# Kernel optimization log

Hardware: AMD Instinct MI355X
Metric: run time of the kernel (lower is better)

The kernel has to match this reference:

```python
import jax, jax.numpy as jnp
import numpy as np

TOP_K = 4
NORM_TOPK_PROB = False  # Qwen2-MoE default

def setup_inputs() -> dict:
    key = jax.random.key(0)
    ks = jax.random.split(key, 10)
    B, S, D = 1, 2048, 2048
    E, F, FS = 8, 1408, 5632
    s = 0.02
    return {
        "hidden_states": jax.random.normal(ks[0], (B, S, D), jnp.float32),
        "gate_w": jax.random.normal(ks[1], (E, D), jnp.float32) * s,          # router Linear weight [E, D]
        "Wg": jax.random.normal(ks[2], (E, D, F), jnp.float32) * s,           # expert gate_proj
        "Wu": jax.random.normal(ks[3], (E, D, F), jnp.float32) * s,           # expert up_proj
        "Wd": jax.random.normal(ks[4], (E, F, D), jnp.float32) * s,           # expert down_proj
        "Wsg": jax.random.normal(ks[5], (D, FS), jnp.float32) * s,            # shared gate_proj
        "Wsu": jax.random.normal(ks[6], (D, FS), jnp.float32) * s,            # shared up_proj
        "Wsd": jax.random.normal(ks[7], (FS, D), jnp.float32) * s,            # shared down_proj
        "shared_gate_w": jax.random.normal(ks[8], (D, 1), jnp.float32) * s,   # shared_expert_gate Linear(D,1)
    }

def reference(hidden_states, gate_w, Wg, Wu, Wd, Wsg, Wsu, Wsd, shared_gate_w):
    B, S, D = hidden_states.shape
    x = hidden_states.reshape(-1, D)                       # [T, D]
    T = x.shape[0]
    router_logits = x @ gate_w.T                           # [T, E]
    probs = jax.nn.softmax(router_logits.astype(jnp.float32), axis=-1)
    top_vals, top_idx = jax.lax.top_k(probs, TOP_K)        # [T, K]
    if NORM_TOPK_PROB:
        top_vals = top_vals / jnp.sum(top_vals, axis=-1, keepdims=True)
    # dense routing-weight matrix: zero for unselected experts (same math as masked naive loop)
    w = jnp.zeros_like(probs).at[jnp.arange(T)[:, None], top_idx].set(top_vals)
    w = w.astype(x.dtype)                                  # [T, E]
    # per-expert SiLU-gated MLP, computed densely over all experts
    h = jax.nn.silu(jnp.einsum('td,edf->etf', x, Wg)) * jnp.einsum('td,edf->etf', x, Wu)  # [E, T, F]
    expert_out = jnp.einsum('etf,efd->etd', h, Wd)         # [E, T, D]
    moe_out = jnp.einsum('etd,te->td', expert_out, w)      # [T, D]
    # shared expert with sigmoid gate
    shared = (jax.nn.silu(x @ Wsg) * (x @ Wsu)) @ Wsd      # [T, D]
    shared = jax.nn.sigmoid(x @ shared_gate_w) * shared    # [T,1] * [T,D]
    out = (moe_out + shared).reshape(B, S, D)
    return out, router_logits
```

## Files before the change

### kernel.cpp

```cpp
#include <hip/hip_runtime.h>
#include <hip/hip_bf16.h>

typedef __attribute__((ext_vector_type(8))) __bf16 bf16x8;
typedef __attribute__((ext_vector_type(4))) float f32x4;

#define TKN 2048
#define DMODEL 2048
#define NEXP 8
#define FEXP 1408
#define FSH 5632

__device__ __forceinline__ unsigned short f2bf(float f) {
  unsigned u = __float_as_uint(f);
  u += 0x7FFFu + ((u >> 16) & 1u);
  return (unsigned short)(u >> 16);
}
__device__ __forceinline__ unsigned pk2(float a, float b) {
  return (unsigned)f2bf(a) | ((unsigned)f2bf(b) << 16);
}

__device__ __forceinline__ void gll16(const void* g, void* l) {
  __builtin_amdgcn_global_load_lds(
      (const __attribute__((address_space(1))) unsigned*)g,
      (__attribute__((address_space(3))) unsigned*)l, 16, 0, 0);
}

enum { EPI_GU = 0, EPI_DOWN = 1, EPI_SDOWN = 2 };

__global__ __launch_bounds__(256)
void router_k(const float* __restrict__ x, const float* __restrict__ gw,
              const float* __restrict__ sgw, float* __restrict__ logits,
              float* __restrict__ sig, int* __restrict__ cnt,
              int* __restrict__ tokl, float* __restrict__ wls)
{
  const int wv = threadIdx.x >> 6, lane = threadIdx.x & 63;
  const int t = blockIdx.x * 4 + wv;
  const float* xr = x + (long)t * DMODEL;
  float xv[32];
#pragma unroll
  for (int j = 0; j < 32; j++) xv[j] = xr[lane + (j << 6)];

  float lg[8];
#pragma unroll
  for (int e = 0; e < 8; e++) {
    const float* gr = gw + (long)e * DMODEL;
    float acc = 0.f;
#pragma unroll
    for (int j = 0; j < 32; j++) acc += xv[j] * gr[lane + (j << 6)];
#pragma unroll
    for (int s = 1; s < 64; s <<= 1) acc += __shfl_xor(acc, s, 64);
    lg[e] = acc;
  }
  float sgacc = 0.f;
#pragma unroll
  for (int j = 0; j < 32; j++) sgacc += xv[j] * sgw[lane + (j << 6)];
#pragma unroll
  for (int s = 1; s < 64; s <<= 1) sgacc += __shfl_xor(sgacc, s, 64);

  if (lane == 0) {
    float mx = lg[0];
#pragma unroll
    for (int e = 1; e < 8; e++) mx = fmaxf(mx, lg[e]);
    float p[8], se = 0.f;
#pragma unroll
    for (int e = 0; e < 8; e++) { p[e] = expf(lg[e] - mx); se += p[e]; }
    float inv = 1.f / se;
#pragma unroll
    for (int e = 0; e < 8; e++) { p[e] *= inv; logits[t * 8 + e] = lg[e]; }
    sig[t] = 1.f / (1.f + expf(-sgacc));
#pragma unroll
    for (int k = 0; k < 4; k++) {
      int bi = 0; float bv = p[0];
#pragma unroll
      for (int e = 1; e < 8; e++) if (p[e] > bv) { bv = p[e]; bi = e; }
      p[bi] = -1.f;
      int pos = atomicAdd(&cnt[bi], 1);
      tokl[bi * TKN + pos] = t;
      wls[bi * TKN + pos] = bv;
    }
  }
}

__global__ void scan_k(const int* __restrict__ cnt, int* __restrict__ offs) {
  if (threadIdx.x == 0) {
    int s = 0;
    for (int e = 0; e < 8; e++) { offs[e] = s; s += cnt[e]; }
    offs[8] = s;
  }
}

__global__ __launch_bounds__(256)
void cvt_x_k(const float* __restrict__ x, char* __restrict__ xbf)
{
  long id = (long)blockIdx.x * 256 + threadIdx.x;
  int row = id >> 8, u = id & 255, kt = u >> 2, j = u & 3;
  const float* p = x + (long)row * 2048 + kt * 32 + j * 4;
  float4 a = *(const float4*)p;
  float4 b = *(const float4*)(p + 16);
  uint4 o;
  o.x = pk2(a.x, a.y); o.y = pk2(a.z, a.w);
  o.z = pk2(b.x, b.y); o.w = pk2(b.z, b.w);
  *(uint4*)(xbf + id * 16) = o;
}

__global__ __launch_bounds__(256)
void cvt_w_k(const float* __restrict__ W, long sB, int N,
             char* __restrict__ panel, long panStride)
{
  const int ct = blockIdx.x, kt = blockIdx.y, e = blockIdx.z, KT = gridDim.y;
  const float* Wp = W + (long)e * sB + (long)(kt * 32) * N + ct * 128;
  __shared__ float t[32][128];
  const int r = threadIdx.x >> 3, q = threadIdx.x & 7;
  const float* rp = Wp + (long)r * N + q * 16;
  float4 f0 = *(const float4*)(rp + 0);
  float4 f1 = *(const float4*)(rp + 4);
  float4 f2 = *(const float4*)(rp + 8);
  float4 f3 = *(const float4*)(rp + 12);
  *(float4*)&t[r][q * 16 + 0]  = f0;
  *(float4*)&t[r][q * 16 + 4]  = f1;
  *(float4*)&t[r][q * 16 + 8]  = f2;
  *(float4*)&t[r][q * 16 + 12] = f3;
  __syncthreads();
  char* outp = panel + e * panStride + ((long)ct * KT + kt) * 8192;
#pragma unroll
  for (int uu = 0; uu < 2; uu++) {
    int u = threadIdx.x + uu * 256;
    int c = u >> 2, g = u & 3;
    uint4 o;
    o.x = pk2(t[g * 4 + 0][c], t[g * 4 + 1][c]);
    o.y = pk2(t[g * 4 + 2][c], t[g * 4 + 3][c]);
    o.z = pk2(t[16 + g * 4 + 0][c], t[16 + g * 4 + 1][c]);
    o.w = pk2(t[16 + g * 4 + 2][c], t[16 + g * 4 + 3][c]);
    *(uint4*)(outp + u * 16) = o;
  }
}

template<int EPI, bool EXPERT, int KSPLIT>
__global__ __launch_bounds__(256, 2)
void gemm2_k(const char* __restrict__ Abf, long strA,
             const char* __restrict__ Bp, const char* __restrict__ Bp2,
             long sBpan, int KTtot,
             void* __restrict__ O, int ldKo,
             const int* __restrict__ cnt, const int* __restrict__ offs,
             const int* __restrict__ tokl, const float* __restrict__ wls,
             const float* __restrict__ sig)
{
  constexpr bool FUSED = (EPI == EPI_GU);
  const int tid = threadIdx.x, lane = tid & 63, w = tid >> 6;

  int e = 0, rt, kc = 0, M = TKN;
  if (EXPERT) {
    e = blockIdx.y >> 4; rt = blockIdx.y & 15;
    M = cnt[e];
    if (rt * 128 >= M) return;
  } else {
    rt = blockIdx.y & 15; kc = blockIdx.y >> 4;
  }
  const int KT = KTtot / KSPLIT;
  const int kt0 = kc * KT;
  const int ct = blockIdx.x;
  const int obase = EXPERT ? offs[e] : 0;

  __shared__ int s_tok[128];
  __shared__ float s_w[128];
  __shared__ alignas(16) char Ab[2][8192];
  __shared__ alignas(16) char Bb[2][8192];
  __shared__ alignas(16) char Bb2[FUSED ? 2 : 1][FUSED ? 8192 : 16];

  if (EXPERT) {
    if (tid < 128) {
      int r = rt * 128 + tid;
      int rc = (r < M) ? r : (M - 1);
      s_tok[tid] = tokl[e * TKN + rc];
      if (EPI == EPI_DOWN) s_w[tid] = (r < M) ? wls[e * TKN + r] : 0.f;
    }
    __syncthreads();
  }

  const int lrow0 = w * 32 + (lane >> 2);
  const int lrow1 = lrow0 + 16;
  auto rowbyte = [&](int rl) -> long {
    long gr;
    if (EPI == EPI_DOWN) { int r = rt * 128 + rl; gr = obase + ((r < M) ? r : (M - 1)); }
    else if (EXPERT)     { gr = s_tok[rl]; }
    else                 { gr = rt * 128 + rl; }
    return gr * strA;
  };
  const char* gA0 = Abf + rowbyte(lrow0) + (long)kt0 * 64 + (lane & 3) * 16;
  const char* gA1 = Abf + rowbyte(lrow1) + (long)kt0 * 64 + (lane & 3) * 16;
  const long bbase = (EXPERT ? (long)e * sBpan : 0) + ((long)ct * KTtot + kt0) * 8192
                     + w * 2048 + (long)lane * 16;
  const char* gB  = Bp + bbase;
  const char* gB2 = FUSED ? (Bp2 + bbase) : nullptr;

  auto stage = [&](int bf, int kt) {
    long ao = (long)kt * 64, bo = (long)kt * 8192;
    gll16(gA0 + ao, &Ab[bf][w * 2048]);
    gll16(gA1 + ao, &Ab[bf][w * 2048 + 1024]);
    gll16(gB + bo, &Bb[bf][w * 2048]);
    gll16(gB + bo + 1024, &Bb[bf][w * 2048 + 1024]);
    if constexpr (FUSED) {
      gll16(gB2 + bo, &Bb2[bf][w * 2048]);
      gll16(gB2 + bo + 1024, &Bb2[bf][w * 2048 + 1024]);
    }
  };

  const int wm = w >> 1, wn = w & 1, g = lane >> 4, l15 = lane & 15;
  int raOff[4], rbOff[4];
#pragma unroll
  for (int m = 0; m < 4; m++) raOff[m] = (wm * 64 + m * 16 + l15) * 64 + g * 16;
#pragma unroll
  for (int n = 0; n < 4; n++) rbOff[n] = (wn * 64 + n * 16 + l15) * 64 + g * 16;

  f32x4 acc[4][4] = {};
  f32x4 acc2[4][4] = {};

  stage(0, 0);
  asm volatile("s_waitcnt vmcnt(0)" ::: "memory");
  __builtin_amdgcn_s_barrier();
  __builtin_amdgcn_sched_barrier(0);

  int bf = 0;
#pragma unroll 1
  for (int kt = 0; kt < KT; ++kt) {
    if (kt + 1 < KT) stage(bf ^ 1, kt + 1);
    bf16x8 av[4], bg[4], bu[4];
#pragma unroll
    for (int m = 0; m < 4; m++) av[m] = *(const bf16x8*)&Ab[bf][raOff[m]];
#pragma unroll
    for (int n = 0; n < 4; n++) {
      bg[n] = *(const bf16x8*)&Bb[bf][rbOff[n]];
      if constexpr (FUSED) bu[n] = *(const bf16x8*)&Bb2[bf][rbOff[n]];
    }
    __builtin_amdgcn_s_setprio(1);
#pragma unroll
    for (int m = 0; m < 4; m++)
#pragma unroll
      for (int n = 0; n < 4; n++) {
        acc[m][n] = __builtin_amdgcn_mfma_f32_16x16x32_bf16(av[m], bg[n], acc[m][n], 0, 0, 0);
        if constexpr (FUSED)
          acc2[m][n] = __builtin_amdgcn_mfma_f32_16x16x32_bf16(av[m], bu[n], acc2[m][n], 0, 0, 0);
      }
    __builtin_amdgcn_s_setprio(0);
    __builtin_amdgcn_sched_barrier(0);
    asm volatile("s_waitcnt vmcnt(0)" ::: "memory");
    __builtin_amdgcn_s_barrier();
    __builtin_amdgcn_sched_barrier(0);
    bf ^= 1;
  }

#pragma unroll
  for (int m = 0; m < 4; m++) {
#pragma unroll
    for (int n = 0; n < 4; n++) {
      int col = ct * 128 + wn * 64 + n * 16 + l15;
      f32x4 a = acc[m][n];
      f32x4 a2 = acc2[m][n];
#pragma unroll
      for (int q = 0; q < 4; q++) {
        int rl = wm * 64 + m * 16 + (g << 2) + q;
        int grow = rt * 128 + rl;
        float v = a[q];
        if constexpr (EPI == EPI_GU) {
          if (!EXPERT || grow < M) {
            float hv = (v / (1.f + __expf(-v))) * a2[q];
            long byteoff = (long)(obase + grow) * ((long)ldKo * 64)
                         + (col >> 5) * 64 + ((col >> 2) & 3) * 16
                         + ((col & 16) >> 1) + (col & 3) * 2;
            *(unsigned short*)((char*)O + byteoff) = f2bf(hv);
          }
        } else if constexpr (EPI == EPI_DOWN) {
          if (grow < M)
            atomicAdd((float*)O + (long)s_tok[rl] * DMODEL + col, s_w[rl] * v);
        } else {
          atomicAdd((float*)O + (long)grow * DMODEL + col, sig[grow] * v);
        }
      }
    }
  }
}

__device__ __forceinline__ void block_sync_fb() {
  __builtin_amdgcn_sched_barrier(0);
  asm volatile("s_waitcnt lgkmcnt(0)" ::: "memory");
  __builtin_amdgcn_s_barrier();
  __builtin_amdgcn_sched_barrier(0);
}

template<int EPI, bool EXPERT, int KSPLIT>
__global__ __launch_bounds__(256, 2)
void gemm_fb_k(const float* __restrict__ A, int lda,
               const float* __restrict__ B, const float* __restrict__ B2,
               long sB, int ldb, int Ktot,
               float* __restrict__ O, int ldo,
               const int* __restrict__ cnt, const int* __restrict__ offs,
               const int* __restrict__ tokl, const float* __restrict__ wls,
               const float* __restrict__ sig)
{
  constexpr bool FUSED = (EPI == EPI_GU);
  const int tid = threadIdx.x;
  const int lane = tid & 63;

  int e = 0, rt, kc = 0, M = TKN;
  if (EXPERT) {
    e = blockIdx.y >> 4; rt = blockIdx.y & 15;
    M = cnt[e];
    if (rt * 128 >= M) return;
  } else {
    rt = blockIdx.y & 15; kc = blockIdx.y >> 4;
  }
  const int K = Ktot / KSPLIT;
  const int koff = kc * K;
  const int colblk = blockIdx.x * 128;
  const float* Bp  = B + (EXPERT ? (long)e * sB : 0);
  const float* Bp2 = FUSED ? (B2 + (EXPERT ? (long)e * sB : 0)) : nullptr;
  const int obase = EXPERT ? offs[e] : 0;

  __shared__ alignas(16) unsigned char Ab[8192];
  __shared__ alignas(16) unsigned char Bb[8192];
  __shared__ alignas(16) unsigned char Bb2[FUSED ? 8192 : 16];
  __shared__ int s_tok[128];
  __shared__ float s_w[128];

  if (EXPERT && tid < 128) {
    int r = rt * 128 + tid;
    int rc = (r < M) ? r : (M - 1);
    s_tok[tid] = tokl[e * TKN + rc];
    if (EPI == EPI_DOWN) s_w[tid] = (r < M) ? wls[e * TKN + r] : 0.f;
  }
  if (EXPERT) __syncthreads();

  const int arowl = tid >> 1;
  const int ahalf = tid & 1;
  long arow;
  if (EPI == EPI_DOWN) {
    int r = rt * 128 + arowl;
    arow = (long)obase + ((r < M) ? r : (M - 1));
  } else if (EXPERT) {
    arow = s_tok[arowl];
  } else {
    arow = rt * 128 + arowl;
  }
  const float* aptr = A + arow * (long)lda + koff + ahalf * 16;
  int wa[4];
#pragma unroll
  for (int j = 0; j < 4; j++)
    wa[j] = arowl * 64 + ((j ^ ((arowl ^ (arowl >> 3)) & 3)) << 4) + ahalf * 8;

  const int kg = tid >> 5, ng = tid & 31;
  const float* bptr  = Bp + (long)(koff + kg * 4) * ldb + colblk + ng * 4;
  const float* bptr2 = FUSED ? (Bp2 + (long)(koff + kg * 4) * ldb + colblk + ng * 4) : nullptr;
  int wb[4];
#pragma unroll
  for (int i = 0; i < 4; i++) {
    int c = ng * 4 + i;
    wb[i] = c * 64 + ((((kg & 3) ^ ((c ^ (c >> 3)) & 3))) << 4) + (kg >> 2) * 8;
  }

  const int wid = tid >> 6, wm = wid >> 1, wn = wid & 1;
  const int g = lane >> 4, l15 = lane & 15;
  int ra[4], rb[4];
#pragma unroll
  for (int m = 0; m < 4; m++) {
    int r = wm * 64 + m * 16 + l15;
    ra[m] = r * 64 + ((g ^ ((r ^ (r >> 3)) & 3)) << 4);
  }
#pragma unroll
  for (int n = 0; n < 4; n++) {
    int c = wn * 64 + n * 16 + l15;
    rb[n] = c * 64 + ((g ^ ((c ^ (c >> 3)) & 3)) << 4);
  }

  f32x4 acc[4][4] = {};
  f32x4 acc2[4][4] = {};

  const int KT = K >> 5;
  float4 ta0[4], tb0[4], tc0[4], ta1[4], tb1[4], tc1[4];

  auto load_tile = [&](float4* ra_, float4* rb_, float4* rc_, int kt) {
    const float4* a4 = reinterpret_cast<const float4*>(aptr + kt * 32);
    ra_[0] = a4[0]; ra_[1] = a4[1]; ra_[2] = a4[2]; ra_[3] = a4[3];
    const float* bb = bptr + (long)kt * 32 * ldb;
    rb_[0] = *reinterpret_cast<const float4*>(bb);
    rb_[1] = *reinterpret_cast<const float4*>(bb + ldb);
    rb_[2] = *reinterpret_cast<const float4*>(bb + 2 * ldb);
    rb_[3] = *reinterpret_cast<const float4*>(bb + 3 * ldb);
    if (FUSED) {
      const float* cc = bptr2 + (long)kt * 32 * ldb;
      rc_[0] = *reinterpret_cast<const float4*>(cc);
      rc_[1] = *reinterpret_cast<const float4*>(cc + ldb);
      rc_[2] = *reinterpret_cast<const float4*>(cc + 2 * ldb);
      rc_[3] = *reinterpret_cast<const float4*>(cc + 3 * ldb);
    }
  };

  auto store_tile = [&](const float4* ra_, const float4* rb_, const float4* rc_) {
#pragma unroll
    for (int j = 0; j < 4; j++)
      *reinterpret_cast<uint2*>(Ab + wa[j]) =
          make_uint2(pk2(ra_[j].x, ra_[j].y), pk2(ra_[j].z, ra_[j].w));
    *reinterpret_cast<uint2*>(Bb + wb[0]) = make_uint2(pk2(rb_[0].x, rb_[1].x), pk2(rb_[2].x, rb_[3].x));
    *reinterpret_cast<uint2*>(Bb + wb[1]) = make_uint2(pk2(rb_[0].y, rb_[1].y), pk2(rb_[2].y, rb_[3].y));
    *reinterpret_cast<uint2*>(Bb + wb[2]) = make_uint2(pk2(rb_[0].z, rb_[1].z), pk2(rb_[2].z, rb_[3].z));
    *reinterpret_cast<uint2*>(Bb + wb[3]) = make_uint2(pk2(rb_[0].w, rb_[1].w), pk2(rb_[2].w, rb_[3].w));
    if (FUSED) {
      *reinterpret_cast<uint2*>(Bb2 + wb[0]) = make_uint2(pk2(rc_[0].x, rc_[1].x), pk2(rc_[2].x, rc_[3].x));
      *reinterpret_cast<uint2*>(Bb2 + wb[1]) = make_uint2(pk2(rc_[0].y, rc_[1].y), pk2(rc_[2].y, rc_[3].y));
      *reinterpret_cast<uint2*>(Bb2 + wb[2]) = make_uint2(pk2(rc_[0].z, rc_[1].z), pk2(rc_[2].z, rc_[3].z));
      *reinterpret_cast<uint2*>(Bb2 + wb[3]) = make_uint2(pk2(rc_[0].w, rc_[1].w), pk2(rc_[2].w, rc_[3].w));
    }
  };

  auto mfma_step = [&]() {
    bf16x8 av[4], bvg[4], bvu[4];
#pragma unroll
    for (int m = 0; m < 4; m++) av[m] = *reinterpret_cast<const bf16x8*>(Ab + ra[m]);
#pragma unroll
    for (int n = 0; n < 4; n++) {
      bvg[n] = *reinterpret_cast<const bf16x8*>(Bb + rb[n]);
      if (FUSED) bvu[n] = *reinterpret_cast<const bf16x8*>(Bb2 + rb[n]);
    }
#pragma unroll
    for (int m = 0; m < 4; m++)
#pragma unroll
      for (int n = 0; n < 4; n++) {
        acc[m][n] = __builtin_amdgcn_mfma_f32_16x16x32_bf16(av[m], bvg[n], acc[m][n], 0, 0, 0);
        if (FUSED)
          acc2[m][n] = __builtin_amdgcn_mfma_f32_16x16x32_bf16(av[m], bvu[n], acc2[m][n], 0, 0, 0);
      }
  };

  load_tile(ta0, tb0, tc0, 0);
#pragma unroll 1
  for (int kt = 0; kt < KT; kt += 2) {
    load_tile(ta1, tb1, tc1, kt + 1);
    store_tile(ta0, tb0, tc0);
    block_sync_fb();
    mfma_step();
    block_sync_fb();
    int k2 = (kt + 2 < KT) ? kt + 2 : 0;
    load_tile(ta0, tb0, tc0, k2);
    store_tile(ta1, tb1, tc1);
    block_sync_fb();
    mfma_step();
    block_sync_fb();
  }

#pragma unroll
  for (int m = 0; m < 4; m++) {
#pragma unroll
    for (int n = 0; n < 4; n++) {
      int col = colblk + wn * 64 + n * 16 + l15;
      f32x4 a = acc[m][n];
      f32x4 a2 = acc2[m][n];
#pragma unroll
      for (int q = 0; q < 4; q++) {
        int rl = wm * 64 + m * 16 + (g << 2) + q;
        int grow = rt * 128 + rl;
        float v = a[q];
        if (EPI == EPI_GU) {
          if (!EXPERT || grow < M) {
            float hv = (v / (1.f + __expf(-v))) * a2[q];
            O[(long)(obase + grow) * ldo + col] = hv;
          }
        } else if (EPI == EPI_DOWN) {
          if (grow < M)
            atomicAdd(&O[(long)s_tok[rl] * ldo + col], s_w[rl] * v);
        } else {
          atomicAdd(&O[(long)grow * ldo + col], sig[grow] * v);
        }
      }
    }
  }
}

extern "C" void kernel_launch(void* const* d_in, const int* in_sizes, int n_in,
                              void* d_out, int out_size, void* d_ws, size_t ws_size,
                              hipStream_t stream)
{
  (void)in_sizes; (void)n_in; (void)out_size;
  const float* x   = (const float*)d_in[0];
  const float* gw  = (const float*)d_in[1];
  const float* Wg  = (const float*)d_in[2];
  const float* Wu  = (const float*)d_in[3];
  const float* Wd  = (const float*)d_in[4];
  const float* Wsg = (const float*)d_in[5];
  const float* Wsu = (const float*)d_in[6];
  const float* Wsd = (const float*)d_in[7];
  const float* sgw = (const float*)d_in[8];

  float* out    = (float*)d_out;
  float* logits = out + (long)TKN * DMODEL;

  char* w    = (char*)d_ws;
  int*  cnt  = (int*)w;
  int*  offs = (int*)(w + 64);
  float* sig = (float*)(w + 1024);
  int*  tokl = (int*)(w + 16384);
  float* wls = (float*)(w + 81920);

  hipMemsetAsync(out, 0, (size_t)TKN * DMODEL * 4, stream);
  hipMemsetAsync(cnt, 0, 64, stream);

  router_k<<<dim3(TKN / 4), 256, 0, stream>>>(x, gw, sgw, logits, sig, cnt, tokl, wls);
  scan_k<<<1, 64, 0, stream>>>(cnt, offs);

  const size_t NEED = 241172480ull;
  if (ws_size >= NEED) {
    char* xbf   = w + 262144;
    char* h     = w + 8650752;
    char* pan   = w + 33554432;
    char* panWg  = pan;
    char* panWu  = pan + 46137344;
    char* panWd  = pan + 92274688;
    char* panWsg = pan + 138412032;
    char* panWsu = pan + 161480704;
    char* panWsd = pan + 184549376;
    const long sPan = 5767168;

    cvt_x_k<<<dim3(2048), 256, 0, stream>>>(x, xbf);
    cvt_w_k<<<dim3(11, 64, 8), 256, 0, stream>>>(Wg, (long)DMODEL * FEXP, FEXP, panWg, sPan);
    cvt_w_k<<<dim3(11, 64, 8), 256, 0, stream>>>(Wu, (long)DMODEL * FEXP, FEXP, panWu, sPan);
    cvt_w_k<<<dim3(16, 44, 8), 256, 0, stream>>>(Wd, (long)FEXP * DMODEL, DMODEL, panWd, sPan);
    cvt_w_k<<<dim3(44, 64, 1), 256, 0, stream>>>(Wsg, 0, FSH, panWsg, 0);
    cvt_w_k<<<dim3(44, 64, 1), 256, 0, stream>>>(Wsu, 0, FSH, panWsu, 0);
    cvt_w_k<<<dim3(16, 176, 1), 256, 0, stream>>>(Wsd, 0, DMODEL, panWsd, 0);

    gemm2_k<EPI_GU, true, 1><<<dim3(11, 128), 256, 0, stream>>>(
        xbf, 4096, panWg, panWu, sPan, 64, h, 44, cnt, offs, tokl, wls, nullptr);
    gemm2_k<EPI_DOWN, true, 1><<<dim3(16, 128), 256, 0, stream>>>(
        h, 2816, panWd, nullptr, sPan, 44, out, 0, cnt, offs, tokl, wls, nullptr);
    gemm2_k<EPI_GU, false, 1><<<dim3(44, 16), 256, 0, stream>>>(
        xbf, 4096, panWsg, panWsu, 0, 64, h, 176, nullptr, nullptr, nullptr, nullptr, nullptr);
    gemm2_k<EPI_SDOWN, false, 4><<<dim3(16, 64), 256, 0, stream>>>(
        h, 11264, panWsd, nullptr, 0, 176, out, 0, nullptr, nullptr, nullptr, nullptr, sig);
  } else {
    float* h = (float*)(w + (1 << 20));
    gemm_fb_k<EPI_GU, true, 1><<<dim3(FEXP / 128, 128), 256, 0, stream>>>(
        x, DMODEL, Wg, Wu, (long)DMODEL * FEXP, FEXP, DMODEL, h, FEXP, cnt, offs, tokl, wls, nullptr);
    gemm_fb_k<EPI_DOWN, true, 1><<<dim3(DMODEL / 128, 128), 256, 0, stream>>>(
        h, FEXP, Wd, nullptr, (long)FEXP * DMODEL, DMODEL, FEXP, out, DMODEL, cnt, offs, tokl, wls, nullptr);
    gemm_fb_k<EPI_GU, false, 1><<<dim3(FSH / 128, TKN / 128), 256, 0, stream>>>(
        x, DMODEL, Wsg, Wsu, 0, FSH, DMODEL, h, FSH, nullptr, nullptr, nullptr, nullptr, nullptr);
    gemm_fb_k<EPI_SDOWN, false, 4><<<dim3(DMODEL / 128, (TKN / 128) * 4), 256, 0, stream>>>(
        h, FSH, Wsd, nullptr, 0, DMODEL, FSH, out, DMODEL, nullptr, nullptr, nullptr, nullptr, sig);
  }
}
```

Before: 766.7 us.

## Triple-buffer GEMM LDS pipeline and remap grid to 1D for cache locality

The GEMM main loop goes from a double-buffered LDS pipeline with a full vmcnt(0) drain each iteration to a triple-buffered one. Loads are issued two tiles ahead and a partial vmcnt wait lets the next tile's loads stay in flight during the MFMAs. The launch grid also becomes 1D with the expert/row-tile index varying fastest, so blocks that share a weight column tile run close together and should reuse it in L2. The cost is that LDS use grows by half, which may hurt occupancy for the fused kernel (about 72KB per block), and the vmcnt counts are hardcoded to the number of loads per stage.

Result: faster. 695.9 us (-9.2%).

```diff
diff --git a/kernel.cpp b/kernel.cpp
--- a/kernel.cpp
+++ b/kernel.cpp
@@ -139,7 +139,7 @@
 __global__ __launch_bounds__(256, 2)
 void gemm2_k(const char* __restrict__ Abf, long strA,
              const char* __restrict__ Bp, const char* __restrict__ Bp2,
-             long sBpan, int KTtot,
+             long sBpan, int KTtot, int NCT,
              void* __restrict__ O, int ldKo,
              const int* __restrict__ cnt, const int* __restrict__ offs,
              const int* __restrict__ tokl, const float* __restrict__ wls,
@@ -147,25 +147,25 @@
 {
   constexpr bool FUSED = (EPI == EPI_GU);
   const int tid = threadIdx.x, lane = tid & 63, w = tid >> 6;
-
-  int e = 0, rt, kc = 0, M = TKN;
+  const int wg = blockIdx.x;
+
+  int e = 0, rt, ct, kc = 0, M = TKN;
   if (EXPERT) {
-    e = blockIdx.y >> 4; rt = blockIdx.y & 15;
+    e = wg & 7; int q = wg >> 3; rt = q & 15; ct = q >> 4;
     M = cnt[e];
     if (rt * 128 >= M) return;
   } else {
-    rt = blockIdx.y & 15; kc = blockIdx.y >> 4;
+    rt = wg & 15; int q = wg >> 4; ct = q % NCT; kc = q / NCT;
   }
   const int KT = KTtot / KSPLIT;
   const int kt0 = kc * KT;
-  const int ct = blockIdx.x;
   const int obase = EXPERT ? offs[e] : 0;
 
   __shared__ int s_tok[128];
   __shared__ float s_w[128];
-  __shared__ alignas(16) char Ab[2][8192];
-  __shared__ alignas(16) char Bb[2][8192];
-  __shared__ alignas(16) char Bb2[FUSED ? 2 : 1][FUSED ? 8192 : 16];
+  __shared__ alignas(16) char Ab[3][8192];
+  __shared__ alignas(16) char Bb[3][8192];
+  __shared__ alignas(16) char Bb2[FUSED ? 3 : 1][FUSED ? 8192 : 16];
 
   if (EXPERT) {
     if (tid < 128) {
@@ -216,22 +216,32 @@
   f32x4 acc2[4][4] = {};
 
   stage(0, 0);
-  asm volatile("s_waitcnt vmcnt(0)" ::: "memory");
-  __builtin_amdgcn_s_barrier();
-  __builtin_amdgcn_sched_barrier(0);
-
-  int bf = 0;
+  stage(1, 1);
+
+  int rd = 0;
 #pragma unroll 1
   for (int kt = 0; kt < KT; ++kt) {
-    if (kt + 1 < KT) stage(bf ^ 1, kt + 1);
+    if (kt + 1 < KT) {
+      if constexpr (FUSED) asm volatile("s_waitcnt vmcnt(6)" ::: "memory");
+      else                 asm volatile("s_waitcnt vmcnt(4)" ::: "memory");
+    } else {
+      asm volatile("s_waitcnt vmcnt(0)" ::: "memory");
+    }
+    __builtin_amdgcn_s_barrier();
+    __builtin_amdgcn_sched_barrier(0);
+
     bf16x8 av[4], bg[4], bu[4];
 #pragma unroll
-    for (int m = 0; m < 4; m++) av[m] = *(const bf16x8*)&Ab[bf][raOff[m]];
+    for (int m = 0; m < 4; m++) av[m] = *(const bf16x8*)&Ab[rd][raOff[m]];
 #pragma unroll
     for (int n = 0; n < 4; n++) {
-      bg[n] = *(const bf16x8*)&Bb[bf][rbOff[n]];
-      if constexpr (FUSED) bu[n] = *(const bf16x8*)&Bb2[bf][rbOff[n]];
-    }
+      bg[n] = *(const bf16x8*)&Bb[rd][rbOff[n]];
+      if constexpr (FUSED) bu[n] = *(const bf16x8*)&Bb2[rd][rbOff[n]];
+    }
+
+    int wr = rd + 2; if (wr >= 3) wr -= 3;
+    if (kt + 2 < KT) stage(wr, kt + 2);
+
     __builtin_amdgcn_s_setprio(1);
 #pragma unroll
     for (int m = 0; m < 4; m++)
@@ -243,10 +253,7 @@
       }
     __builtin_amdgcn_s_setprio(0);
     __builtin_amdgcn_sched_barrier(0);
-    asm volatile("s_waitcnt vmcnt(0)" ::: "memory");
-    __builtin_amdgcn_s_barrier();
-    __builtin_amdgcn_sched_barrier(0);
-    bf ^= 1;
+    rd = (rd == 2) ? 0 : rd + 1;
   }
 
 #pragma unroll
@@ -526,14 +533,14 @@
     cvt_w_k<<<dim3(44, 64, 1), 256, 0, stream>>>(Wsu, 0, FSH, panWsu, 0);
     cvt_w_k<<<dim3(16, 176, 1), 256, 0, stream>>>(Wsd, 0, DMODEL, panWsd, 0);
 
-    gemm2_k<EPI_GU, true, 1><<<dim3(11, 128), 256, 0, stream>>>(
-        xbf, 4096, panWg, panWu, sPan, 64, h, 44, cnt, offs, tokl, wls, nullptr);
-    gemm2_k<EPI_DOWN, true, 1><<<dim3(16, 128), 256, 0, stream>>>(
-        h, 2816, panWd, nullptr, sPan, 44, out, 0, cnt, offs, tokl, wls, nullptr);
-    gemm2_k<EPI_GU, false, 1><<<dim3(44, 16), 256, 0, stream>>>(
-        xbf, 4096, panWsg, panWsu, 0, 64, h, 176, nullptr, nullptr, nullptr, nullptr, nullptr);
-    gemm2_k<EPI_SDOWN, false, 4><<<dim3(16, 64), 256, 0, stream>>>(
-        h, 11264, panWsd, nullptr, 0, 176, out, 0, nullptr, nullptr, nullptr, nullptr, sig);
+    gemm2_k<EPI_GU, true, 1><<<dim3(8 * 16 * 11), 256, 0, stream>>>(
+        xbf, 4096, panWg, panWu, sPan, 64, 11, h, 44, cnt, offs, tokl, wls, nullptr);
+    gemm2_k<EPI_DOWN, true, 1><<<dim3(8 * 16 * 16), 256, 0, stream>>>(
+        h, 2816, panWd, nullptr, sPan, 44, 16, out, 0, cnt, offs, tokl, wls, nullptr);
+    gemm2_k<EPI_GU, false, 1><<<dim3(16 * 44), 256, 0, stream>>>(
+        xbf, 4096, panWsg, panWsu, 0, 64, 44, h, 176, nullptr, nullptr, nullptr, nullptr, nullptr);
+    gemm2_k<EPI_SDOWN, false, 4><<<dim3(16 * 16 * 4), 256, 0, stream>>>(
+        h, 11264, panWsd, nullptr, 0, 176, 16, out, 0, nullptr, nullptr, nullptr, nullptr, sig);
   } else {
     float* h = (float*)(w + (1 << 20));
     gemm_fb_k<EPI_GU, true, 1><<<dim3(FEXP / 128, 128), 256, 0, stream>>>(
```
